# Kernel optimization log

Hardware: AMD Instinct MI355X
Metric: run time of the kernel (lower is better)

Reference implementation:

```python
import jax, jax.numpy as jnp
import numpy as np

D_MODEL = 1024
H = 4
DK = 128   # head_qk_dim (key_dim=512)
DV = 256   # head_v_dim (value_dim=1024)
EPS = 1e-5
SCALE = DK ** -0.5


def setup_inputs() -> dict:
    key = jax.random.key(0)
    ks = jax.random.split(key, 8)
    w = lambda k, i, o: jax.random.normal(k, (i, o), jnp.float32) * (2.0 ** -2.5) * (6.0 / (i + o)) ** 0.5 * 2
    return {
        "x": jax.random.normal(ks[0], (2, 4096, D_MODEL), jnp.float32),
        "Wq": w(ks[1], D_MODEL, H * DK),
        "Wk": w(ks[2], D_MODEL, H * DK),
        "Wv": w(ks[3], D_MODEL, H * DV),
        "Wb": w(ks[4], D_MODEL, H),
        "Wg": w(ks[5], D_MODEL, H * DV),
        "Wo": w(ks[6], H * DV, D_MODEL),
        "norm_w": jnp.ones((DV,), jnp.float32),
    }


def _delta_rule(q, k, v, beta):
    """Delta-rule linear attention. q,k: [b,n,h,dk], v: [b,n,h,dv], beta: [b,n,h].
    S_t = S_{t-1} + k_t (beta_t * (v_t - k_t^T S_{t-1}))^T ; o_t = q_t^T S_t."""
    b = q.shape[0]
    # time-major for scan: [n,b,h,*]
    qt = jnp.moveaxis(q, 1, 0)
    kt = jnp.moveaxis(k, 1, 0)
    vt = jnp.moveaxis(v, 1, 0)
    bt = jnp.moveaxis(beta, 1, 0)
    S0 = jnp.zeros((b, H, DK, DV), q.dtype)

    def step(S, inp):
        q_t, k_t, v_t, b_t = inp
        pred = jnp.einsum('bhk,bhkv->bhv', k_t, S)          # current memory readout
        delta = (v_t - pred) * b_t[..., None]                # beta-scaled error
        S = S + k_t[..., :, None] * delta[..., None, :]      # rank-1 update [b,h,dk,dv]
        o_t = jnp.einsum('bhk,bhkv->bhv', q_t, S)
        return S, o_t

    _, o = jax.lax.scan(step, S0, (qt, kt, vt, bt))          # o: [n,b,h,dv]
    return jnp.moveaxis(o, 0, 1)                             # [b,n,h,dv]


def reference(x, Wq, Wk, Wv, Wb, Wg, Wo, norm_w):
    b, n, _ = x.shape
    q = (x @ Wq).reshape(b, n, H, DK)
    k = (x @ Wk).reshape(b, n, H, DK)
    v = (x @ Wv).reshape(b, n, H, DV)
    beta = jax.nn.sigmoid(x @ Wb)                            # [b,n,h]
    # L2-normalize keys (delta-rule kernels assume unit-norm k) and scale q
    k = k * jax.lax.rsqrt(jnp.sum(k * k, axis=-1, keepdims=True) + 1e-12)
    q = q * SCALE
    o = _delta_rule(q, k, v, beta)                           # [b,n,h,dv]
    # FusedRMSNormSwishGate over head_v_dim
    g = (x @ Wg).reshape(b, n, H, DV)
    o = o * jax.lax.rsqrt(jnp.mean(o * o, axis=-1, keepdims=True) + EPS) * norm_w
    o = o * (g * jax.nn.sigmoid(g))                          # swish gate
    return o.reshape(b, n, H * DV) @ Wo
```

## Files before the change

kernel.cpp:

```cpp
#include <hip/hip_runtime.h>
#include <hip/hip_bf16.h>
#include <stdint.h>
#include <stddef.h>

typedef __attribute__((ext_vector_type(8))) short short8v;
typedef __attribute__((ext_vector_type(4))) float f32x4;
typedef unsigned short us;

__device__ __forceinline__ float bf2f(unsigned short u) {
    return __uint_as_float(((unsigned int)u) << 16);
}
__device__ __forceinline__ unsigned short f2bf(float f) {
    unsigned int x = __float_as_uint(f);
    x += 0x7fffu + ((x >> 16) & 1u);
    return (unsigned short)(x >> 16);
}
__device__ __forceinline__ unsigned int cvtpk(float lo, float hi) {
    unsigned int r;
    asm("v_cvt_pk_bf16_f32 %0, %1, %2" : "=v"(r) : "v"(lo), "v"(hi));
    return r;
}

#define NTOK 8192
#define DM   1024
#define NPROJ 3072
#define SEQ  4096
#define NCHUNK 64
#define SCQ 0.08838834764831845f

#define GLDS16(g, l) __builtin_amdgcn_global_load_lds( \
    (const __attribute__((address_space(1))) void*)(g), \
    (__attribute__((address_space(3))) void*)(l), 16, 0, 0)

__device__ __forceinline__ void bar_lgkm() {
    asm volatile("s_waitcnt lgkmcnt(0)" ::: "memory");
    __builtin_amdgcn_s_barrier();
    __builtin_amdgcn_sched_barrier(0);
}

__device__ __forceinline__ int sw16(int row, int k) {
    int u = k >> 3;
    int us_ = (u & 8) | ((u ^ row) & 7);
    return row * 128 + us_ * 8 + (k & 7);
}
__device__ __forceinline__ int sw8(int row, int k) {
    int u = k >> 3;
    int us_ = (u ^ row) & 7;
    return row * 64 + us_ * 8 + (k & 7);
}
__device__ __forceinline__ int sw128(int row, int k) {
    int u = k >> 3;
    return row * 128 + ((u ^ row) & 15) * 8 + (k & 7);
}
__device__ __forceinline__ int sw64(int row, int k) {
    int u = k >> 3;
    return row * 64 + ((u ^ row) & 7) * 8 + (k & 7);
}
__device__ __forceinline__ int sw64b(int row, int k) {
    int u = k >> 3;
    return row * 64 + ((u ^ row ^ (row >> 3)) & 7) * 8 + (k & 7);
}
__device__ __forceinline__ int swU(int t, int j) {
    int jj = j & 127, u = jj >> 3;
    int us_ = (u & 8) | ((u ^ t) & 7);
    return t * 256 + (j >> 7) * 128 + us_ * 8 + (jj & 7);
}
__device__ __forceinline__ int swU128(int t, int jj) {
    int u = jj >> 3;
    int us_ = (u & 8) | ((u ^ t) & 7);
    return t * 128 + us_ * 8 + (jj & 7);
}
__device__ __forceinline__ int sw64h(int row, int k) {
    int u = k >> 3;
    return row * 64 + ((u ^ row) & 7) * 8 + (k & 7);
}

__global__ void convert_x(const float* __restrict__ x, us* __restrict__ xb, int nunits) {
    int i = blockIdx.x * 256 + threadIdx.x;
    if (i >= nunits) return;
    int tok = i >> 7;
    int kb = (i >> 3) & 15;
    int u = i & 7;
    int ko = kb * 64 + ((u ^ (tok & 7)) * 8);
    const float4* src = (const float4*)(x + (size_t)tok * 1024 + ko);
    float4 v0 = src[0], v1 = src[1];
    uint4 o;
    o.x = cvtpk(v0.x, v0.y); o.y = cvtpk(v0.z, v0.w);
    o.z = cvtpk(v1.x, v1.y); o.w = cvtpk(v1.z, v1.w);
    *(uint4*)(xb + (size_t)i * 8) = o;
}

__global__ __launch_bounds__(256) void transpose_w(const float* __restrict__ src,
                                                   us* __restrict__ dst, int K, int N) {
    __shared__ float tl[64][65];
    int k0 = blockIdx.y * 64, n0 = blockIdx.x * 64;
    int tid = threadIdx.x;
    int tr = tid >> 6, tc = tid & 63;
    #pragma unroll
    for (int i = 0; i < 16; i++) {
        int kk = 4 * i + tr;
        tl[kk][tc] = src[(size_t)(k0 + kk) * N + n0 + tc];
    }
    __syncthreads();
    int n = tid >> 2, seg = (tid & 3) * 16;
    short8v a, b;
    #pragma unroll
    for (int e = 0; e < 8; e++) {
        a[e] = (short)f2bf(tl[seg + e][n]);
        b[e] = (short)f2bf(tl[seg + 8 + e][n]);
    }
    int n_ = n0 + n;
    int o1 = (tid & 3) * 2, o2_ = o1 + 1;
    us* d = dst + (size_t)n_ * K + k0;
    *(short8v*)(d + (o1 ^ (n_ & 7)) * 8) = a;
    *(short8v*)(d + (o2_ ^ (n_ & 7)) * 8) = b;
}

__global__ __launch_bounds__(256) void beta_kernel(const float* __restrict__ x,
                                                   const float* __restrict__ Wb,
                                                   float* __restrict__ beta) {
    __shared__ float part[16][16][4];
    int tl = threadIdx.x >> 4, sg = threadIdx.x & 15;
    int tok = blockIdx.x * 16 + tl;
    const float4* xr = (const float4*)(x + (size_t)tok * DM);
    const float4* wb = (const float4*)Wb;
    float s0 = 0.f, s1 = 0.f, s2 = 0.f, s3 = 0.f;
    #pragma unroll
    for (int it = 0; it < 16; it++) {
        int f = it * 16 + sg;
        float4 xv = xr[f];
        float4 w0 = wb[4 * f + 0], w1 = wb[4 * f + 1], w2 = wb[4 * f + 2], w3 = wb[4 * f + 3];
        s0 += xv.x * w0.x + xv.y * w1.x + xv.z * w2.x + xv.w * w3.x;
        s1 += xv.x * w0.y + xv.y * w1.y + xv.z * w2.y + xv.w * w3.y;
        s2 += xv.x * w0.z + xv.y * w1.z + xv.z * w2.z + xv.w * w3.z;
        s3 += xv.x * w0.w + xv.y * w1.w + xv.z * w2.w + xv.w * w3.w;
    }
    part[tl][sg][0] = s0; part[tl][sg][1] = s1; part[tl][sg][2] = s2; part[tl][sg][3] = s3;
    __syncthreads();
    if (threadIdx.x < 64) {
        int tl2 = threadIdx.x >> 2, h = threadIdx.x & 3;
        float s = 0.f;
        #pragma unroll
        for (int g = 0; g < 16; g++) s += part[tl2][g][h];
        beta[(size_t)(blockIdx.x * 16 + tl2) * 4 + h] = 1.f / (1.f + __expf(-s));
    }
}

template<int OUT_F32>
__global__ __launch_bounds__(256) void gemm_bt(
    const us* __restrict__ A, const us* __restrict__ BT,
    void* __restrict__ C, int M, int N, int K)
{
    __shared__ us As[128][64];
    __shared__ us Bs[128][64];
    int tid = threadIdx.x;
    int wave = tid >> 6, lane = tid & 63;
    int wr = (wave >> 1) * 64, wc = (wave & 1) * 64;
    int fr = lane & 15, fq = lane >> 4;
    int nbx = gridDim.x, nwg = nbx * gridDim.y;
    int wg = blockIdx.y * nbx + blockIdx.x;
    int cpx = nwg >> 3;
    wg = (wg & 7) * cpx + (wg >> 3);
    int m0 = (wg % nbx) * 128, n0 = (wg / nbx) * 128;

    f32x4 acc[4][4];
    #pragma unroll
    for (int i = 0; i < 4; i++)
        #pragma unroll
        for (int j = 0; j < 4; j++) acc[i][j] = (f32x4){0.f, 0.f, 0.f, 0.f};

    int rl = lane >> 3, ul = lane & 7;

    for (int k0 = 0; k0 < K; k0 += 64) {
        #pragma unroll
        for (int i = 0; i < 4; i++) {
            int row = wave * 32 + i * 8 + rl;
            GLDS16(&A[(size_t)(m0 + row) * K + k0 + ul * 8], &As[0][0] + (wave * 32 + i * 8) * 64);
            GLDS16(&BT[(size_t)(n0 + row) * K + k0 + ul * 8], &Bs[0][0] + (wave * 32 + i * 8) * 64);
        }
        __syncthreads();
        #pragma unroll
        for (int kk = 0; kk < 2; kk++) {
            short8v a[4], b[4];
            #pragma unroll
            for (int i = 0; i < 4; i++) {
                int ra = wr + i * 16 + fr;
                a[i] = *(const short8v*)&As[ra][((4 * kk + fq) ^ (ra & 7)) * 8];
                int rb = wc + i * 16 + fr;
                b[i] = *(const short8v*)&Bs[rb][((4 * kk + fq) ^ (rb & 7)) * 8];
            }
            #pragma unroll
            for (int i = 0; i < 4; i++)
                #pragma unroll
                for (int j = 0; j < 4; j++)
                    acc[i][j] = __builtin_amdgcn_mfma_f32_16x16x32_bf16(a[i], b[j], acc[i][j], 0, 0, 0);
        }
        __syncthreads();
    }
    #pragma unroll
    for (int i = 0; i < 4; i++)
        #pragma unroll
        for (int j = 0; j < 4; j++)
            #pragma unroll
            for (int t = 0; t < 4; t++) {
                int row = m0 + wr + i * 16 + fq * 4 + t;
                int col = n0 + wc + j * 16 + fr;
                float val = acc[i][j][t];
                if (OUT_F32) ((float*)C)[(size_t)row * N + col] = val;
                else ((us*)C)[(size_t)row * N + col] = f2bf(val);
            }
}

__global__ __launch_bounds__(256) void chunk_pre(
    const us* __restrict__ QKVG, const float* __restrict__ beta,
    us* __restrict__ Wbuf, us* __restrict__ Ubuf,
    us* __restrict__ Pbuf, us* __restrict__ KTbuf)
{
    __shared__ us Ks[8192];
    __shared__ us KTs[8192];
    __shared__ us VT[8192];
    __shared__ us Tb[4096];
    __shared__ float Af[64][64];
    __shared__ float betas[64];

    int c = blockIdx.x, bh = blockIdx.y;
    int b = bh >> 2, h = bh & 3;
    int tid = threadIdx.x;
    int wv = tid >> 6, ln = tid & 63;
    int fr = ln & 15, fq = ln >> 4;
    int tok0 = b * SEQ + c * 64;
    size_t cb = (size_t)bh * NCHUNK + c;

    #pragma unroll
    for (int r = 0; r < 4; r++) {
        int idx = tid + 256 * r;
        int t = idx >> 4, u = idx & 15;
        short8v kv = *(const short8v*)(QKVG + (size_t)(tok0 + t) * NPROJ + 512 + h * 128 + u * 8);
        *(short8v*)(Ks + sw16(t, u * 8)) = kv;
    }
    if (tid < 64) betas[tid] = beta[(size_t)(tok0 + tid) * 4 + h];
    __syncthreads();

    {
        int t = tid >> 2, p = tid & 3;
        short8v v[4];
        float ss = 0.f;
        #pragma unroll
        for (int uu = 0; uu < 4; uu++) {
            v[uu] = *(const short8v*)(Ks + sw16(t, (p * 4 + uu) * 8));
            #pragma unroll
            for (int e = 0; e < 8; e++) {
                float f = bf2f((unsigned short)v[uu][e]);
                ss += f * f;
            }
        }
        ss += __shfl_xor(ss, 1);
        ss += __shfl_xor(ss, 2);
        float rn = rsqrtf(ss + 1e-12f);
        #pragma unroll
        for (int uu = 0; uu < 4; uu++) {
            short8v o;
            #pragma unroll
            for (int e = 0; e < 8; e++)
                o[e] = (short)f2bf(bf2f((unsigned short)v[uu][e]) * rn);
            *(short8v*)(Ks + sw16(t, (p * 4 + uu) * 8)) = o;
        }
    }
    __syncthreads();

    {
        f32x4 aacc[4];
        #pragma unroll
        for (int jt = 0; jt < 4; jt++) aacc[jt] = (f32x4){0.f, 0.f, 0.f, 0.f};
        #pragma unroll
        for (int ks = 0; ks < 4; ks++) {
            short8v ak = *(const short8v*)(Ks + sw16(16 * wv + fr, 32 * ks + 8 * fq));
            #pragma unroll
            for (int jt = 0; jt < 4; jt++) {
                short8v bk = *(const short8v*)(Ks + sw16(16 * jt + fr, 32 * ks + 8 * fq));
                aacc[jt] = __builtin_amdgcn_mfma_f32_16x16x32_bf16(ak, bk, aacc[jt], 0, 0, 0);
            }
        }
        #pragma unroll
        for (int jt = 0; jt < 4; jt++)
            #pragma unroll
            for (int r = 0; r < 4; r++) {
                int t = 16 * wv + 4 * fq + r, s = 16 * jt + fr;
                if (s < t) Af[t][s] = betas[t] * aacc[jt][r];
            }
    }
    __syncthreads();

    if (wv == 0) {
        int cc = ln;
        for (int tb = 0; tb < 8; tb++) {
            int base = tb * 8;
            float xs[8];
            #pragma unroll
            for (int i = 0; i < 8; i++) {
                int t = base + i;
                float v = Af[t][cc];
                #pragma unroll
                for (int s = 0; s < i; s++)
                    v += Af[t][base + s] * xs[s];
                float xt = (cc < t) ? -v : 0.f;
                xs[i] = xt;
                if (cc < t) Af[t][cc] = xt;
            }
            for (int r = base + 8; r < 64; r += 2) {
                float u0 = 0.f, u1 = 0.f;
                #pragma unroll
                for (int s = 0; s < 8; s++) {
                    float a0 = Af[r][base + s];
                    float a1 = Af[r + 1][base + s];
                    u0 += a0 * xs[s];
                    u1 += a1 * xs[s];
                }
                Af[r][cc] += u0;
                Af[r + 1][cc] += u1;
            }
        }
    } else {
        int q = tid - 64;
        for (int g = q; g < 1024; g += 192) {
            int t = g >> 4, u = g & 15;
            short8v kv = *(const short8v*)(Ks + sw16(t, u * 8));
            #pragma unroll
            for (int e = 0; e < 8; e++)
                KTs[sw64b(u * 8 + e, t)] = (unsigned short)kv[e];
        }
        for (int g = q; g < 1024; g += 192) {
            int t = g >> 4, jg = g & 15;
            short8v vv = *(const short8v*)(QKVG + (size_t)(tok0 + t) * NPROJ + 1024 + h * 256 + jg * 8);
            #pragma unroll
            for (int e = 0; e < 8; e++)
                VT[sw64b(jg * 8 + e, t)] = (unsigned short)vv[e];
        }
    }
    __syncthreads();

    {
        f32x4 pacc[4];
        #pragma unroll
        for (int jt = 0; jt < 4; jt++) pacc[jt] = (f32x4){0.f, 0.f, 0.f, 0.f};
        #pragma unroll
        for (int ks = 0; ks < 4; ks++) {
            short8v aq = *(const short8v*)(QKVG + (size_t)(tok0 + 16 * wv + fr) * NPROJ + h * 128 + ks * 32 + fq * 8);
            #pragma unroll
            for (int jt = 0; jt < 4; jt++) {
                short8v bk = *(const short8v*)(Ks + sw16(16 * jt + fr, 32 * ks + 8 * fq));
                pacc[jt] = __builtin_amdgcn_mfma_f32_16x16x32_bf16(aq, bk, pacc[jt], 0, 0, 0);
            }
        }
        #pragma unroll
        for (int jt = 0; jt < 4; jt++)
            #pragma unroll
            for (int r = 0; r < 4; r++) {
                int t = 16 * wv + 4 * fq + r, s = 16 * jt + fr;
                float val = (s <= t) ? pacc[jt][r] * SCQ : 0.f;
                Pbuf[cb * 4096 + sw64(t, s)] = f2bf(val);
            }
        #pragma unroll
        for (int i = 0; i < 16; i++) {
            int idx = tid + 256 * i;
            int t = idx >> 6, s = idx & 63;
            float tv = (s < t) ? Af[t][s] : (s == t ? 1.f : 0.f);
            Tb[sw8(t, s)] = f2bf(tv * betas[s]);
        }
        #pragma unroll
        for (int i = 0; i < 4; i++) {
            int idx = tid + 256 * i;
            *(short8v*)(KTbuf + cb * 8192 + (size_t)idx * 8) =
                *(const short8v*)(KTs + (size_t)idx * 8);
        }
    }
    __syncthreads();

    {
        f32x4 wacc[8], uacc[8];
        #pragma unroll
        for (int jt = 0; jt < 8; jt++) {
            wacc[jt] = (f32x4){0.f, 0.f, 0.f, 0.f};
            uacc[jt] = (f32x4){0.f, 0.f, 0.f, 0.f};
        }
        #pragma unroll
        for (int ks = 0; ks < 2; ks++) {
            short8v at = *(const short8v*)(Tb + sw8(16 * wv + fr, 32 * ks + 8 * fq));
            #pragma unroll
            for (int jt = 0; jt < 8; jt++) {
                short8v bk = *(const short8v*)(KTs + sw64b(16 * jt + fr, 32 * ks + 8 * fq));
                wacc[jt] = __builtin_amdgcn_mfma_f32_16x16x32_bf16(at, bk, wacc[jt], 0, 0, 0);
                short8v bv = *(const short8v*)(VT + sw64b(16 * jt + fr, 32 * ks + 8 * fq));
                uacc[jt] = __builtin_amdgcn_mfma_f32_16x16x32_bf16(at, bv, uacc[jt], 0, 0, 0);
            }
        }
        #pragma unroll
        for (int jt = 0; jt < 8; jt++)
            #pragma unroll
            for (int r = 0; r < 4; r++) {
                int t = 16 * wv + 4 * fq + r, d = 16 * jt + fr;
                Wbuf[cb * 8192 + sw128(t, d)] = f2bf(-wacc[jt][r]);
                Ubuf[cb * 16384 + swU(t, d)] = f2bf(uacc[jt][r]);
            }
    }
    __syncthreads();

    #pragma unroll
    for (int i = 0; i < 4; i++) {
        int g = tid + 256 * i;
        int t = g >> 4, jg = g & 15;
        short8v vv = *(const short8v*)(QKVG + (size_t)(tok0 + t) * NPROJ + 1024 + h * 256 + 128 + jg * 8);
        #pragma unroll
        for (int e = 0; e < 8; e++)
            VT[sw64b(jg * 8 + e, t)] = (unsigned short)vv[e];
    }
    __syncthreads();
    {
        f32x4 uacc[8];
        #pragma unroll
        for (int jt = 0; jt < 8; jt++) uacc[jt] = (f32x4){0.f, 0.f, 0.f, 0.f};
        #pragma unroll
        for (int ks = 0; ks < 2; ks++) {
            short8v at = *(const short8v*)(Tb + sw8(16 * wv + fr, 32 * ks + 8 * fq));
            #pragma unroll
            for (int jt = 0; jt < 8; jt++) {
                short8v bv = *(const short8v*)(VT + sw64b(16 * jt + fr, 32 * ks + 8 * fq));
                uacc[jt] = __builtin_amdgcn_mfma_f32_16x16x32_bf16(at, bv, uacc[jt], 0, 0, 0);
            }
        }
        #pragma unroll
        for (int jt = 0; jt < 8; jt++)
            #pragma unroll
            for (int r = 0; r < 4; r++) {
                int t = 16 * wv + 4 * fq + r, j = 16 * jt + fr;
                Ubuf[cb * 16384 + swU(t, 128 + j)] = f2bf(uacc[jt][r]);
            }
    }
}

#define SCW 0
#define SCKT 8192
#define SCU 16384
#define SCBUF 17408
#define SCST 34816
#define SCDT 36864
#define SCPXB 77824

__global__ __launch_bounds__(128, 1) void scan_mfma(
    const us* __restrict__ Wbuf, const us* __restrict__ Ubuf,
    const us* __restrict__ KTbuf, us* __restrict__ Sbuf)
{
    extern __shared__ us lds[];
    float* pxf = (float*)((char*)lds + SCPXB);
    int tid = threadIdx.x;
    int wv = tid >> 6, ln = tid & 63;
    int fr = ln & 15, fq = ln >> 4;
    int sl = blockIdx.x;
    int j0 = sl * 16;
    int bh = blockIdx.y;

    short8v id0;
    #pragma unroll
    for (int e = 0; e < 8; e++)
        id0[e] = (short)((8 * fq + e == fr) ? 0x3F80 : 0);

    f32x4 sacc[4];
    #pragma unroll
    for (int i = 0; i < 4; i++) sacc[i] = (f32x4){0.f, 0.f, 0.f, 0.f};

    us* ST = lds + SCST + wv * 1024;
    us* DT = lds + SCDT + wv * 1024;

    auto issue = [&](int c1) {
        size_t cb = (size_t)bh * NCHUNK + c1;
        us* dst = lds + (c1 & 1) * SCBUF;
        const us* Wc = Wbuf + cb * 8192;
        const us* Kc = KTbuf + cb * 8192;
        #pragma unroll
        for (int i = 0; i < 8; i++) {
            int p = wv * 8 + i;
            GLDS16(Wc + p * 512 + ln * 8, dst + SCW + p * 512);
            GLDS16(Kc + wv * 4096 + i * 512 + ln * 8, dst + SCKT + wv * 4096 + i * 512);
        }
        const us* Uc = Ubuf + cb * 16384;
        int t = wv * 32 + (ln >> 1);
        GLDS16(Uc + swU(t, j0 + (ln & 1) * 8), dst + SCU + wv * 512);
    };

    issue(0);

    for (int c = 0; c < NCHUNK; c++) {
        const us* ba = lds + (c & 1) * SCBUF;

        #pragma unroll
        for (int dt = 0; dt < 4; dt++) {
            uint2 w;
            w.x = cvtpk(sacc[dt][0], sacc[dt][1]);
            w.y = cvtpk(sacc[dt][2], sacc[dt][3]);
            int dl = 16 * dt + 4 * fq;
            *(uint2*)&ST[fr * 64 + (((dl >> 3) ^ fr) & 7) * 8 + (dl & 7)] = w;
        }
        if (c + 1 < NCHUNK) issue(c + 1);
        {
            size_t sb = ((size_t)bh * NCHUNK + c) * 32768 + sl * 2048 + wv * 1024;
            #pragma unroll
            for (int q = 0; q < 2; q++) {
                short8v v = *(const short8v*)&ST[q * 512 + ln * 8];
                *(short8v*)(Sbuf + sb + q * 512 + ln * 8) = v;
            }
        }
        if (c + 1 < NCHUNK) {
            asm volatile("s_waitcnt vmcnt(19)" ::: "memory");
        } else {
            asm volatile("s_waitcnt vmcnt(4)" ::: "memory");
        }
        __builtin_amdgcn_sched_barrier(0);
        __builtin_amdgcn_s_barrier();
        __builtin_amdgcn_sched_barrier(0);

        f32x4 dacc[4];
        #pragma unroll
        for (int tt = 0; tt < 4; tt++) dacc[tt] = (f32x4){0.f, 0.f, 0.f, 0.f};
        #pragma unroll
        for (int kc = 0; kc < 2; kc++) {
            short8v bs = *(const short8v*)&ST[fr * 64 + (((4 * kc + fq) ^ fr) & 7) * 8];
            #pragma unroll
            for (int tt = 0; tt < 4; tt++) {
                short8v aw = *(const short8v*)&ba[SCW + sw128(16 * tt + fr, 64 * wv + 32 * kc + 8 * fq)];
                dacc[tt] = __builtin_amdgcn_mfma_f32_16x16x32_bf16(aw, bs, dacc[tt], 0, 0, 0);
            }
        }
        if (wv) {
            #pragma unroll
            for (int tt = 0; tt < 4; tt++) {
                short8v au = *(const short8v*)&ba[SCU + (16 * tt + fr) * 16 + 8 * (fq & 1)];
                dacc[tt] = __builtin_amdgcn_mfma_f32_16x16x32_bf16(au, id0, dacc[tt], 0, 0, 0);
            }
        }
        #pragma unroll
        for (int tt = 0; tt < 4; tt++)
            *(f32x4*)&pxf[wv * 1024 + tt * 256 + ln * 4] = dacc[tt];
        bar_lgkm();
        #pragma unroll
        for (int tt = 0; tt < 4; tt++) {
            f32x4 o = *(const f32x4*)&pxf[(wv ^ 1) * 1024 + tt * 256 + ln * 4];
            dacc[tt] += o;
        }
        #pragma unroll
        for (int tt = 0; tt < 4; tt++) {
            uint2 w;
            w.x = cvtpk(dacc[tt][0], dacc[tt][1]);
            w.y = cvtpk(dacc[tt][2], dacc[tt][3]);
            int tl = 16 * tt + 4 * fq;
            *(uint2*)&DT[fr * 64 + (((tl >> 3) ^ fr) & 7) * 8 + (tl & 7)] = w;
        }
        #pragma unroll
        for (int kc2 = 0; kc2 < 2; kc2++) {
            short8v bd = *(const short8v*)&DT[fr * 64 + (((4 * kc2 + fq) ^ fr) & 7) * 8];
            #pragma unroll
            for (int dt = 0; dt < 4; dt++) {
                short8v ak = *(const short8v*)&ba[SCKT + sw64b(64 * wv + 16 * dt + fr, 32 * kc2 + 8 * fq)];
                sacc[dt] = __builtin_amdgcn_mfma_f32_16x16x32_bf16(ak, bd, sacc[dt], 0, 0, 0);
            }
        }
    }
}

#define K2_W 0
#define K2_P 8192
#define K2_U 12288
#define K2_S 20480
#define K2_Q 36864
#define K2_DT 45056

__global__ __launch_bounds__(256, 1) void out_k(
    const us* __restrict__ QKVG, const us* __restrict__ Wbuf,
    const us* __restrict__ Ubuf, const us* __restrict__ Pbuf,
    const us* __restrict__ Sbuf, us* __restrict__ Ob)
{
    extern __shared__ us lds[];
    int tid = threadIdx.x;
    int wv = tid >> 6, ln = tid & 63;
    int fr = ln & 15, fq = ln >> 4;
    int c = blockIdx.x;
    int bh = blockIdx.y >> 1, jh = blockIdx.y & 1;
    int b = bh >> 2, h = bh & 3;
    int tok0 = b * SEQ + c * 64;
    size_t cb = (size_t)bh * NCHUNK + c;

    short8v id0, id1;
    #pragma unroll
    for (int e = 0; e < 8; e++) {
        id0[e] = (short)((8 * fq + e == fr) ? 0x3F80 : 0);
        id1[e] = (short)((8 * fq + e == fr + 16) ? 0x3F80 : 0);
    }

    #pragma unroll
    for (int i = 0; i < 4; i++) {
        int q = (i * 4 + wv) * 512 + ln * 8;
        GLDS16(Wbuf + cb * 8192 + q, lds + K2_W + (i * 4 + wv) * 512);
    }
    #pragma unroll
    for (int i = 0; i < 2; i++) {
        int q = (i * 4 + wv) * 512 + ln * 8;
        GLDS16(Pbuf + cb * 4096 + q, lds + K2_P + (i * 4 + wv) * 512);
    }
    #pragma unroll
    for (int i = 0; i < 4; i++) {
        int q = (i * 4 + wv) * 512 + ln * 8;
        int t = q >> 7, r = q & 127;
        GLDS16(Ubuf + cb * 16384 + t * 256 + jh * 128 + r, lds + K2_U + (i * 4 + wv) * 512);
    }
    size_t sbase = cb * 32768 + (size_t)jh * 16384;
    #pragma unroll
    for (int i = 0; i < 8; i++) {
        int q = (i * 4 + wv) * 512 + ln * 8;
        GLDS16(Sbuf + sbase + q, lds + K2_S + (i * 4 + wv) * 512);
    }
    short8v qv[4];
    #pragma unroll
    for (int i = 0; i < 4; i++) {
        int idx = tid + 256 * i;
        int t = idx >> 4, u = idx & 15;
        qv[i] = *(const short8v*)(QKVG + (size_t)(tok0 + t) * NPROJ + h * 128 + u * 8);
    }
    #pragma unroll
    for (int i = 0; i < 4; i++) {
        int idx = tid + 256 * i;
        int t = idx >> 4, u = idx & 15;
        *(short8v*)&lds[K2_Q + sw128(t, u * 8)] = qv[i];
    }
    __syncthreads();

    f32x4 dacc[8], oacc[8];
    #pragma unroll
    for (int jt = 0; jt < 8; jt++) {
        dacc[jt] = (f32x4){0.f, 0.f, 0.f, 0.f};
        oacc[jt] = (f32x4){0.f, 0.f, 0.f, 0.f};
    }
    #pragma unroll
    for (int ks = 0; ks < 4; ks++) {
        short8v aw = *(const short8v*)&lds[K2_W + sw128(16 * wv + fr, 32 * ks + 8 * fq)];
        short8v aq = *(const short8v*)&lds[K2_Q + sw128(16 * wv + fr, 32 * ks + 8 * fq)];
        #pragma unroll
        for (int jt = 0; jt < 8; jt++) {
            short8v bs = *(const short8v*)&lds[K2_S + jt * 2048 + (ks >> 1) * 1024
                + fr * 64 + ((((ks & 1) * 4 + fq) ^ fr) & 7) * 8];
            dacc[jt] = __builtin_amdgcn_mfma_f32_16x16x32_bf16(aw, bs, dacc[jt], 0, 0, 0);
            oacc[jt] = __builtin_amdgcn_mfma_f32_16x16x32_bf16(aq, bs, oacc[jt], 0, 0, 0);
        }
    }
    #pragma unroll
    for (int ju = 0; ju < 4; ju++) {
        short8v au = *(const short8v*)&lds[K2_U + swU128(16 * wv + fr, 32 * ju + 8 * fq)];
        dacc[2 * ju + 0] = __builtin_amdgcn_mfma_f32_16x16x32_bf16(au, id0, dacc[2 * ju + 0], 0, 0, 0);
        dacc[2 * ju + 1] = __builtin_amdgcn_mfma_f32_16x16x32_bf16(au, id1, dacc[2 * ju + 1], 0, 0, 0);
    }
    #pragma unroll
    for (int jt = 0; jt < 8; jt++)
        #pragma unroll
        for (int r = 0; r < 4; r++) oacc[jt][r] *= SCQ;
    #pragma unroll
    for (int jt = 0; jt < 8; jt++) {
        int j = 16 * jt + fr;
        int t0 = 16 * wv + 4 * fq;
        uint2 w;
        w.x = cvtpk(dacc[jt][0], dacc[jt][1]);
        w.y = cvtpk(dacc[jt][2], dacc[jt][3]);
        *(uint2*)&lds[K2_DT + sw64(j, t0)] = w;
    }
    bar_lgkm();

    #pragma unroll
    for (int ks = 0; ks < 2; ks++) {
        short8v ap = *(const short8v*)&lds[K2_P + sw64(16 * wv + fr, 32 * ks + 8 * fq)];
        #pragma unroll
        for (int jt = 0; jt < 8; jt++) {
            short8v bd = *(const short8v*)&lds[K2_DT + sw64(16 * jt + fr, 32 * ks + 8 * fq)];
            oacc[jt] = __builtin_amdgcn_mfma_f32_16x16x32_bf16(ap, bd, oacc[jt], 0, 0, 0);
        }
    }
    us* ob = Ob + (size_t)tok0 * 1024 + h * 256 + jh * 128;
    #pragma unroll
    for (int jt = 0; jt < 8; jt++)
        #pragma unroll
        for (int r = 0; r < 4; r++) {
            int t = 16 * wv + 4 * fq + r;
            ob[(size_t)t * 1024 + 16 * jt + fr] = f2bf(oacc[jt][r]);
        }
}

__global__ __launch_bounds__(256) void gate_norm(const us* __restrict__ Ob,
                                                 const us* __restrict__ QKVG,
                                                 const float* __restrict__ norm_w,
                                                 us* __restrict__ o2)
{
    int gid = blockIdx.x * 4 + (threadIdx.x >> 6);
    int ln = threadIdx.x & 63;
    int tok = gid >> 2, h = gid & 3;
    size_t base = (size_t)tok * 1024 + h * 256 + ln * 4;
    uint2 ov = *(const uint2*)&Ob[base];
    float o0 = bf2f((us)ov.x), o1 = bf2f((us)(ov.x >> 16));
    float o2v = bf2f((us)ov.y), o3 = bf2f((us)(ov.y >> 16));
    float ss = o0 * o0 + o1 * o1 + o2v * o2v + o3 * o3;
    #pragma unroll
    for (int off = 32; off; off >>= 1) ss += __shfl_xor(ss, off);
    float r = rsqrtf(ss * (1.0f / 256.0f) + 1e-5f);
    uint2 gv = *(const uint2*)&QKVG[(size_t)tok * NPROJ + 2048 + h * 256 + ln * 4];
    float g0 = bf2f((us)gv.x), g1 = bf2f((us)(gv.x >> 16));
    float g2 = bf2f((us)gv.y), g3 = bf2f((us)(gv.y >> 16));
    float4 nw = *(const float4*)&norm_w[ln * 4];
    float r0 = o0 * r * nw.x * (g0 / (1.f + __expf(-g0)));
    float r1 = o1 * r * nw.y * (g1 / (1.f + __expf(-g1)));
    float r2 = o2v * r * nw.z * (g2 / (1.f + __expf(-g2)));
    float r3 = o3 * r * nw.w * (g3 / (1.f + __expf(-g3)));
    uint2 w;
    w.x = cvtpk(r0, r1);
    w.y = cvtpk(r2, r3);
    int u = h * 32 + (ln >> 1);
    size_t dsto = (size_t)tok * 1024 + (size_t)(u >> 3) * 64
                + (size_t)(((u & 7) ^ (tok & 7)) * 8) + (ln & 1) * 4;
    *(uint2*)&o2[dsto] = w;
}

extern "C" void kernel_launch(void* const* d_in, const int* in_sizes, int n_in,
                              void* d_out, int out_size, void* d_ws, size_t ws_size,
                              hipStream_t stream) {
    const float* x      = (const float*)d_in[0];
    const float* Wq     = (const float*)d_in[1];
    const float* Wk     = (const float*)d_in[2];
    const float* Wv     = (const float*)d_in[3];
    const float* Wb     = (const float*)d_in[4];
    const float* Wg     = (const float*)d_in[5];
    const float* Wo     = (const float*)d_in[6];
    const float* norm_w = (const float*)d_in[7];
    float* out = (float*)d_out;

    char* ws = (char*)d_ws;
    us*    xb   = (us*)(ws + 0);
    us*    WT   = (us*)(ws + 16777216);
    us*    Sbuf = (us*)(ws + 0);
    us*    KTbuf= (us*)(ws + 33554432);
    us*    Ob   = (us*)(ws + 33554432);
    us*    QKVG = (us*)(ws + 50331648);
    float* beta = (float*)(ws + 100663296);
    us*    Wbuf = (us*)(ws + 100794368);
    us*    Ubuf = (us*)(ws + 109182976);
    us*    o2   = (us*)(ws + 109182976);
    us*    Pbuf = (us*)(ws + 125960192);
    us*    WoT  = (us*)(ws + 130154496);

    (void)hipFuncSetAttribute((const void*)scan_mfma,
                              hipFuncAttributeMaxDynamicSharedMemorySize, 86016);
    (void)hipFuncSetAttribute((const void*)out_k,
                              hipFuncAttributeMaxDynamicSharedMemorySize, 106496);

    convert_x<<<NTOK * 128 / 256, 256, 0, stream>>>(x, xb, NTOK * 128);
    transpose_w<<<dim3(8, 16), 256, 0, stream>>>(Wq, WT, DM, 512);
    transpose_w<<<dim3(8, 16), 256, 0, stream>>>(Wk, WT + (size_t)512 * DM, DM, 512);
    transpose_w<<<dim3(16, 16), 256, 0, stream>>>(Wv, WT + (size_t)1024 * DM, DM, 1024);
    transpose_w<<<dim3(16, 16), 256, 0, stream>>>(Wg, WT + (size_t)2048 * DM, DM, 1024);
    transpose_w<<<dim3(16, 16), 256, 0, stream>>>(Wo, WoT, DM, 1024);
    beta_kernel<<<NTOK / 16, 256, 0, stream>>>(x, Wb, beta);
    gemm_bt<0><<<dim3(64, 24), 256, 0, stream>>>(xb, WT, (void*)QKVG, NTOK, NPROJ, DM);
    chunk_pre<<<dim3(NCHUNK, 8), 256, 0, stream>>>(QKVG, beta, Wbuf, Ubuf, Pbuf, KTbuf);
    scan_mfma<<<dim3(16, 8), 128, 86016, stream>>>(Wbuf, Ubuf, KTbuf, Sbuf);
    out_k<<<dim3(NCHUNK, 16), 256, 106496, stream>>>(QKVG, Wbuf, Ubuf, Pbuf, Sbuf, Ob);
    gate_norm<<<NTOK, 256, 0, stream>>>(Ob, QKVG, norm_w, o2);
    gemm_bt<1><<<dim3(64, 8), 256, 0, stream>>>(o2, WoT, (void*)out, NTOK, DM, DM);
}
```

Measured before the change: 264.9 us.

## Precompute per-chunk transition matrix to shorten serial scan dependency chain

chunk_pre now also forms a per-chunk 128x128 matrix M = K^T W (stored as Mbuf), plus a transposed U layout, so the scan step becomes S_new = S + K^T U + M S without the intermediate D = W S + U round-trip through LDS and the cross-wave reduction. scan_mfma drops one barrier and the fp32 partial-sum exchange per chunk, writes S directly to global, and double-buffers the state tile. The cost is more work in chunk_pre, a larger Mbuf load per chunk in the scan (more LDS and bandwidth), and a changed grid mapping. out_k is adapted to the transposed U layout.

```diff
diff --git a/kernel.cpp b/kernel.cpp
--- a/kernel.cpp
+++ b/kernel.cpp
@@ -60,19 +60,9 @@
     int u = k >> 3;
     return row * 64 + ((u ^ row ^ (row >> 3)) & 7) * 8 + (k & 7);
 }
-__device__ __forceinline__ int swU(int t, int j) {
-    int jj = j & 127, u = jj >> 3;
-    int us_ = (u & 8) | ((u ^ t) & 7);
-    return t * 256 + (j >> 7) * 128 + us_ * 8 + (jj & 7);
-}
-__device__ __forceinline__ int swU128(int t, int jj) {
-    int u = jj >> 3;
-    int us_ = (u & 8) | ((u ^ t) & 7);
-    return t * 128 + us_ * 8 + (jj & 7);
-}
-__device__ __forceinline__ int sw64h(int row, int k) {
-    int u = k >> 3;
-    return row * 64 + ((u ^ row) & 7) * 8 + (k & 7);
+__device__ __forceinline__ int swUT(int j, int t) {
+    int u = t >> 3;
+    return j * 64 + ((u ^ j) & 7) * 8 + (t & 7);
 }
 
 __global__ void convert_x(const float* __restrict__ x, us* __restrict__ xb, int nunits) {
@@ -213,8 +203,8 @@
 
 __global__ __launch_bounds__(256) void chunk_pre(
     const us* __restrict__ QKVG, const float* __restrict__ beta,
-    us* __restrict__ Wbuf, us* __restrict__ Ubuf,
-    us* __restrict__ Pbuf, us* __restrict__ KTbuf)
+    us* __restrict__ Wbuf, us* __restrict__ UbufT,
+    us* __restrict__ Pbuf, us* __restrict__ KTbuf, us* __restrict__ Mbuf)
 {
     __shared__ us Ks[8192];
     __shared__ us KTs[8192];
@@ -222,6 +212,7 @@
     __shared__ us Tb[4096];
     __shared__ float Af[64][64];
     __shared__ float betas[64];
+    us* WTl = (us*)&Af[0][0];
 
     int c = blockIdx.x, bh = blockIdx.y;
     int b = bh >> 2, h = bh & 3;
@@ -399,8 +390,10 @@
             #pragma unroll
             for (int r = 0; r < 4; r++) {
                 int t = 16 * wv + 4 * fq + r, d = 16 * jt + fr;
-                Wbuf[cb * 8192 + sw128(t, d)] = f2bf(-wacc[jt][r]);
-                Ubuf[cb * 16384 + swU(t, d)] = f2bf(uacc[jt][r]);
+                us wneg = f2bf(-wacc[jt][r]);
+                Wbuf[cb * 8192 + sw128(t, d)] = wneg;
+                WTl[sw64b(d, t)] = wneg;
+                UbufT[cb * 16384 + swUT(d, t)] = f2bf(uacc[jt][r]);
             }
     }
     __syncthreads();
@@ -432,65 +425,81 @@
         for (int jt = 0; jt < 8; jt++)
             #pragma unroll
             for (int r = 0; r < 4; r++) {
-                int t = 16 * wv + 4 * fq + r, j = 16 * jt + fr;
-                Ubuf[cb * 16384 + swU(t, 128 + j)] = f2bf(uacc[jt][r]);
-            }
-    }
-}
-
-#define SCW 0
-#define SCKT 8192
-#define SCU 16384
-#define SCBUF 17408
-#define SCST 34816
-#define SCDT 36864
-#define SCPXB 77824
+                int t = 16 * wv + 4 * fq + r, j = 128 + 16 * jt + fr;
+                UbufT[cb * 16384 + swUT(j, t)] = f2bf(uacc[jt][r]);
+            }
+    }
+
+    {
+        #pragma unroll
+        for (int mw = 0; mw < 2; mw++) {
+            int mt = wv + 4 * mw;
+            f32x4 macc[8];
+            #pragma unroll
+            for (int nt = 0; nt < 8; nt++) macc[nt] = (f32x4){0.f, 0.f, 0.f, 0.f};
+            #pragma unroll
+            for (int ks = 0; ks < 2; ks++) {
+                short8v akt = *(const short8v*)(KTs + sw64b(16 * mt + fr, 32 * ks + 8 * fq));
+                #pragma unroll
+                for (int nt = 0; nt < 8; nt++) {
+                    short8v bwt = *(const short8v*)(WTl + sw64b(16 * nt + fr, 32 * ks + 8 * fq));
+                    macc[nt] = __builtin_amdgcn_mfma_f32_16x16x32_bf16(akt, bwt, macc[nt], 0, 0, 0);
+                }
+            }
+            #pragma unroll
+            for (int nt = 0; nt < 8; nt++)
+                #pragma unroll
+                for (int r = 0; r < 4; r++) {
+                    int d = 16 * mt + 4 * fq + r, dp = 16 * nt + fr;
+                    Mbuf[cb * 16384 + sw128(d, dp)] = f2bf(macc[nt][r]);
+                }
+        }
+    }
+}
+
+#define SMB 0
+#define SKT 16384
+#define SUT 24576
+#define SBUFSZ 25600
+#define SSTB (2 * SBUFSZ)
 
 __global__ __launch_bounds__(128, 1) void scan_mfma(
-    const us* __restrict__ Wbuf, const us* __restrict__ Ubuf,
+    const us* __restrict__ Mbuf, const us* __restrict__ UbufT,
     const us* __restrict__ KTbuf, us* __restrict__ Sbuf)
 {
     extern __shared__ us lds[];
-    float* pxf = (float*)((char*)lds + SCPXB);
     int tid = threadIdx.x;
     int wv = tid >> 6, ln = tid & 63;
     int fr = ln & 15, fq = ln >> 4;
-    int sl = blockIdx.x;
+    int sl = blockIdx.x >> 3;
     int j0 = sl * 16;
-    int bh = blockIdx.y;
-
-    short8v id0;
-    #pragma unroll
-    for (int e = 0; e < 8; e++)
-        id0[e] = (short)((8 * fq + e == fr) ? 0x3F80 : 0);
+    int bh = blockIdx.x & 7;
 
     f32x4 sacc[4];
     #pragma unroll
     for (int i = 0; i < 4; i++) sacc[i] = (f32x4){0.f, 0.f, 0.f, 0.f};
-
-    us* ST = lds + SCST + wv * 1024;
-    us* DT = lds + SCDT + wv * 1024;
 
     auto issue = [&](int c1) {
         size_t cb = (size_t)bh * NCHUNK + c1;
-        us* dst = lds + (c1 & 1) * SCBUF;
-        const us* Wc = Wbuf + cb * 8192;
-        const us* Kc = KTbuf + cb * 8192;
-        #pragma unroll
-        for (int i = 0; i < 8; i++) {
-            int p = wv * 8 + i;
-            GLDS16(Wc + p * 512 + ln * 8, dst + SCW + p * 512);
-            GLDS16(Kc + wv * 4096 + i * 512 + ln * 8, dst + SCKT + wv * 4096 + i * 512);
-        }
-        const us* Uc = Ubuf + cb * 16384;
-        int t = wv * 32 + (ln >> 1);
-        GLDS16(Uc + swU(t, j0 + (ln & 1) * 8), dst + SCU + wv * 512);
+        us* dst = lds + (c1 & 1) * SBUFSZ;
+        const us* Mc = Mbuf + cb * 16384 + wv * 8192;
+        const us* Kc = KTbuf + cb * 8192 + wv * 4096;
+        #pragma unroll
+        for (int i = 0; i < 16; i++)
+            GLDS16(Mc + i * 512 + ln * 8, dst + SMB + wv * 8192 + i * 512);
+        #pragma unroll
+        for (int i = 0; i < 8; i++)
+            GLDS16(Kc + i * 512 + ln * 8, dst + SKT + wv * 4096 + i * 512);
+        GLDS16(UbufT + cb * 16384 + j0 * 64 + wv * 512 + ln * 8, dst + SUT + wv * 512);
     };
 
     issue(0);
 
     for (int c = 0; c < NCHUNK; c++) {
-        const us* ba = lds + (c & 1) * SCBUF;
+        const us* ba = lds + (c & 1) * SBUFSZ;
+        us* STw = lds + SSTB + (c & 1) * 2048 + wv * 1024;
+        const us* STr = lds + SSTB + (c & 1) * 2048;
+        size_t sb = ((size_t)bh * NCHUNK + c) * 32768 + sl * 2048 + wv * 1024;
 
         #pragma unroll
         for (int dt = 0; dt < 4; dt++) {
@@ -498,69 +507,38 @@
             w.x = cvtpk(sacc[dt][0], sacc[dt][1]);
             w.y = cvtpk(sacc[dt][2], sacc[dt][3]);
             int dl = 16 * dt + 4 * fq;
-            *(uint2*)&ST[fr * 64 + (((dl >> 3) ^ fr) & 7) * 8 + (dl & 7)] = w;
+            int off = fr * 64 + (((dl >> 3) ^ fr) & 7) * 8 + (dl & 7);
+            *(uint2*)&STw[off] = w;
+            *(uint2*)(Sbuf + sb + off) = w;
         }
         if (c + 1 < NCHUNK) issue(c + 1);
-        {
-            size_t sb = ((size_t)bh * NCHUNK + c) * 32768 + sl * 2048 + wv * 1024;
-            #pragma unroll
-            for (int q = 0; q < 2; q++) {
-                short8v v = *(const short8v*)&ST[q * 512 + ln * 8];
-                *(short8v*)(Sbuf + sb + q * 512 + ln * 8) = v;
-            }
-        }
-        if (c + 1 < NCHUNK) {
-            asm volatile("s_waitcnt vmcnt(19)" ::: "memory");
+        if (c == 0) {
+            asm volatile("s_waitcnt vmcnt(29)" ::: "memory");
+        } else if (c + 1 < NCHUNK) {
+            asm volatile("s_waitcnt vmcnt(33)" ::: "memory");
         } else {
-            asm volatile("s_waitcnt vmcnt(4)" ::: "memory");
+            asm volatile("s_waitcnt vmcnt(8)" ::: "memory");
         }
         __builtin_amdgcn_sched_barrier(0);
-        __builtin_amdgcn_s_barrier();
-        __builtin_amdgcn_sched_barrier(0);
-
-        f32x4 dacc[4];
-        #pragma unroll
-        for (int tt = 0; tt < 4; tt++) dacc[tt] = (f32x4){0.f, 0.f, 0.f, 0.f};
-        #pragma unroll
-        for (int kc = 0; kc < 2; kc++) {
-            short8v bs = *(const short8v*)&ST[fr * 64 + (((4 * kc + fq) ^ fr) & 7) * 8];
-            #pragma unroll
-            for (int tt = 0; tt < 4; tt++) {
-                short8v aw = *(const short8v*)&ba[SCW + sw128(16 * tt + fr, 64 * wv + 32 * kc + 8 * fq)];
-                dacc[tt] = __builtin_amdgcn_mfma_f32_16x16x32_bf16(aw, bs, dacc[tt], 0, 0, 0);
-            }
-        }
-        if (wv) {
-            #pragma unroll
-            for (int tt = 0; tt < 4; tt++) {
-                short8v au = *(const short8v*)&ba[SCU + (16 * tt + fr) * 16 + 8 * (fq & 1)];
-                dacc[tt] = __builtin_amdgcn_mfma_f32_16x16x32_bf16(au, id0, dacc[tt], 0, 0, 0);
-            }
-        }
-        #pragma unroll
-        for (int tt = 0; tt < 4; tt++)
-            *(f32x4*)&pxf[wv * 1024 + tt * 256 + ln * 4] = dacc[tt];
         bar_lgkm();
-        #pragma unroll
-        for (int tt = 0; tt < 4; tt++) {
-            f32x4 o = *(const f32x4*)&pxf[(wv ^ 1) * 1024 + tt * 256 + ln * 4];
-            dacc[tt] += o;
-        }
-        #pragma unroll
-        for (int tt = 0; tt < 4; tt++) {
-            uint2 w;
-            w.x = cvtpk(dacc[tt][0], dacc[tt][1]);
-            w.y = cvtpk(dacc[tt][2], dacc[tt][3]);
-            int tl = 16 * tt + 4 * fq;
-            *(uint2*)&DT[fr * 64 + (((tl >> 3) ^ fr) & 7) * 8 + (tl & 7)] = w;
-        }
-        #pragma unroll
-        for (int kc2 = 0; kc2 < 2; kc2++) {
-            short8v bd = *(const short8v*)&DT[fr * 64 + (((4 * kc2 + fq) ^ fr) & 7) * 8];
+
+        #pragma unroll
+        for (int ks = 0; ks < 2; ks++) {
+            short8v but = *(const short8v*)&ba[SUT + fr * 64 + (((4 * ks + fq) ^ (fr & 7)) & 7) * 8];
             #pragma unroll
             for (int dt = 0; dt < 4; dt++) {
-                short8v ak = *(const short8v*)&ba[SCKT + sw64b(64 * wv + 16 * dt + fr, 32 * kc2 + 8 * fq)];
-                sacc[dt] = __builtin_amdgcn_mfma_f32_16x16x32_bf16(ak, bd, sacc[dt], 0, 0, 0);
+                short8v akt = *(const short8v*)&ba[SKT + wv * 4096 + sw64b(16 * dt + fr, 32 * ks + 8 * fq)];
+                sacc[dt] = __builtin_amdgcn_mfma_f32_16x16x32_bf16(akt, but, sacc[dt], 0, 0, 0);
+            }
+        }
+        #pragma unroll
+        for (int kc = 0; kc < 4; kc++) {
+            short8v bs = *(const short8v*)&STr[(kc >> 1) * 1024 + fr * 64
+                + ((((kc & 1) * 4 + fq) ^ fr) & 7) * 8];
+            #pragma unroll
+            for (int dt = 0; dt < 4; dt++) {
+                short8v am = *(const short8v*)&ba[SMB + sw128(64 * wv + 16 * dt + fr, 32 * kc + 8 * fq)];
+                sacc[dt] = __builtin_amdgcn_mfma_f32_16x16x32_bf16(am, bs, sacc[dt], 0, 0, 0);
             }
         }
     }
@@ -575,7 +553,7 @@
 
 __global__ __launch_bounds__(256, 1) void out_k(
     const us* __restrict__ QKVG, const us* __restrict__ Wbuf,
-    const us* __restrict__ Ubuf, const us* __restrict__ Pbuf,
+    const us* __restrict__ UbufT, const us* __restrict__ Pbuf,
     const us* __restrict__ Sbuf, us* __restrict__ Ob)
 {
     extern __shared__ us lds[];
@@ -588,12 +566,10 @@
     int tok0 = b * SEQ + c * 64;
     size_t cb = (size_t)bh * NCHUNK + c;
 
-    short8v id0, id1;
-    #pragma unroll
-    for (int e = 0; e < 8; e++) {
-        id0[e] = (short)((8 * fq + e == fr) ? 0x3F80 : 0);
-        id1[e] = (short)((8 * fq + e == fr + 16) ? 0x3F80 : 0);
-    }
+    short8v idw;
+    #pragma unroll
+    for (int e = 0; e < 8; e++)
+        idw[e] = (short)((8 * fq + e == fr + 16 * (wv & 1)) ? 0x3F80 : 0);
 
     #pragma unroll
     for (int i = 0; i < 4; i++) {
@@ -608,8 +584,7 @@
     #pragma unroll
     for (int i = 0; i < 4; i++) {
         int q = (i * 4 + wv) * 512 + ln * 8;
-        int t = q >> 7, r = q & 127;
-        GLDS16(Ubuf + cb * 16384 + t * 256 + jh * 128 + r, lds + K2_U + (i * 4 + wv) * 512);
+        GLDS16(UbufT + cb * 16384 + jh * 8192 + q, lds + K2_U + (i * 4 + wv) * 512);
     }
     size_t sbase = cb * 32768 + (size_t)jh * 16384;
     #pragma unroll
@@ -632,10 +607,10 @@
     }
     __syncthreads();
 
-    f32x4 dacc[8], oacc[8];
+    f32x4 daccT[8], oacc[8];
     #pragma unroll
     for (int jt = 0; jt < 8; jt++) {
-        dacc[jt] = (f32x4){0.f, 0.f, 0.f, 0.f};
+        daccT[jt] = (f32x4){0.f, 0.f, 0.f, 0.f};
         oacc[jt] = (f32x4){0.f, 0.f, 0.f, 0.f};
     }
     #pragma unroll
@@ -646,29 +621,27 @@
         for (int jt = 0; jt < 8; jt++) {
             short8v bs = *(const short8v*)&lds[K2_S + jt * 2048 + (ks >> 1) * 1024
                 + fr * 64 + ((((ks & 1) * 4 + fq) ^ fr) & 7) * 8];
-            dacc[jt] = __builtin_amdgcn_mfma_f32_16x16x32_bf16(aw, bs, dacc[jt], 0, 0, 0);
+            daccT[jt] = __builtin_amdgcn_mfma_f32_16x16x32_bf16(bs, aw, daccT[jt], 0, 0, 0);
             oacc[jt] = __builtin_amdgcn_mfma_f32_16x16x32_bf16(aq, bs, oacc[jt], 0, 0, 0);
         }
     }
     #pragma unroll
-    for (int ju = 0; ju < 4; ju++) {
-        short8v au = *(const short8v*)&lds[K2_U + swU128(16 * wv + fr, 32 * ju + 8 * fq)];
-        dacc[2 * ju + 0] = __builtin_amdgcn_mfma_f32_16x16x32_bf16(au, id0, dacc[2 * ju + 0], 0, 0, 0);
-        dacc[2 * ju + 1] = __builtin_amdgcn_mfma_f32_16x16x32_bf16(au, id1, dacc[2 * ju + 1], 0, 0, 0);
+    for (int jt = 0; jt < 8; jt++) {
+        short8v au = *(const short8v*)&lds[K2_U + (16 * jt + fr) * 64
+            + ((((wv >> 1) * 4 + fq) ^ (fr & 7)) & 7) * 8];
+        daccT[jt] = __builtin_amdgcn_mfma_f32_16x16x32_bf16(au, idw, daccT[jt], 0, 0, 0);
     }
     #pragma unroll
     for (int jt = 0; jt < 8; jt++)
         #pragma unroll
         for (int r = 0; r < 4; r++) oacc[jt][r] *= SCQ;
     #pragma unroll
-    for (int jt = 0; jt < 8; jt++) {
-        int j = 16 * jt + fr;
-        int t0 = 16 * wv + 4 * fq;
-        uint2 w;
-        w.x = cvtpk(dacc[jt][0], dacc[jt][1]);
-        w.y = cvtpk(dacc[jt][2], dacc[jt][3]);
-        *(uint2*)&lds[K2_DT + sw64(j, t0)] = w;
-    }
+    for (int jt = 0; jt < 8; jt++)
+        #pragma unroll
+        for (int r = 0; r < 4; r++) {
+            int j = 16 * jt + 4 * fq + r, t = 16 * wv + fr;
+            lds[K2_DT + sw64(j, t)] = f2bf(daccT[jt][r]);
+        }
     bar_lgkm();
 
     #pragma unroll
@@ -740,18 +713,19 @@
     us*    xb   = (us*)(ws + 0);
     us*    WT   = (us*)(ws + 16777216);
     us*    Sbuf = (us*)(ws + 0);
-    us*    KTbuf= (us*)(ws + 33554432);
+    us*    Mbuf = (us*)(ws + 33554432);
     us*    Ob   = (us*)(ws + 33554432);
     us*    QKVG = (us*)(ws + 50331648);
     float* beta = (float*)(ws + 100663296);
     us*    Wbuf = (us*)(ws + 100794368);
-    us*    Ubuf = (us*)(ws + 109182976);
+    us*    UbufT= (us*)(ws + 109182976);
     us*    o2   = (us*)(ws + 109182976);
     us*    Pbuf = (us*)(ws + 125960192);
     us*    WoT  = (us*)(ws + 130154496);
+    us*    KTbuf= (us*)(ws + 132251648);
 
     (void)hipFuncSetAttribute((const void*)scan_mfma,
-                              hipFuncAttributeMaxDynamicSharedMemorySize, 86016);
+                              hipFuncAttributeMaxDynamicSharedMemorySize, 110592);
     (void)hipFuncSetAttribute((const void*)out_k,
                               hipFuncAttributeMaxDynamicSharedMemorySize, 106496);
 
@@ -763,9 +737,9 @@
     transpose_w<<<dim3(16, 16), 256, 0, stream>>>(Wo, WoT, DM, 1024);
     beta_kernel<<<NTOK / 16, 256, 0, stream>>>(x, Wb, beta);
     gemm_bt<0><<<dim3(64, 24), 256, 0, stream>>>(xb, WT, (void*)QKVG, NTOK, NPROJ, DM);
-    chunk_pre<<<dim3(NCHUNK, 8), 256, 0, stream>>>(QKVG, beta, Wbuf, Ubuf, Pbuf, KTbuf);
-    scan_mfma<<<dim3(16, 8), 128, 86016, stream>>>(Wbuf, Ubuf, KTbuf, Sbuf);
-    out_k<<<dim3(NCHUNK, 16), 256, 106496, stream>>>(QKVG, Wbuf, Ubuf, Pbuf, Sbuf, Ob);
+    chunk_pre<<<dim3(NCHUNK, 8), 256, 0, stream>>>(QKVG, beta, Wbuf, UbufT, Pbuf, KTbuf, Mbuf);
+    scan_mfma<<<128, 128, 110592, stream>>>(Mbuf, UbufT, KTbuf, Sbuf);
+    out_k<<<dim3(NCHUNK, 16), 256, 106496, stream>>>(QKVG, Wbuf, UbufT, Pbuf, Sbuf, Ob);
     gate_norm<<<NTOK, 256, 0, stream>>>(Ob, QKVG, norm_w, o2);
     gemm_bt<1><<<dim3(64, 8), 256, 0, stream>>>(o2, WoT, (void*)out, NTOK, DM, DM);
 }
```

New measurement: 282.1 us. +6.5%, slower.

## Restructure scan kernel's inter-wave reduction to remove a barrier and fp32 exchange

Applied to the files above, without the earlier changes.

Changes the chunk W layout to two 64-column halves so each wave loads only its own half of W and K. The scan now writes both waves' bf16 partial D tiles into double-buffered LDS and lets each wave accumulate both partials with extra MFMAs. This replaces the fp32 partial-sum exchange, the extra barrier and the LDS round trip for the state store, which now goes straight from registers to global. Block indexing is flattened to a 1D grid. The trade-off is twice the MFMAs in the state update, and the partials are rounded to bf16 before they are summed.

```diff
diff --git a/kernel.cpp b/kernel.cpp
--- a/kernel.cpp
+++ b/kernel.cpp
@@ -69,10 +69,6 @@
     int u = jj >> 3;
     int us_ = (u & 8) | ((u ^ t) & 7);
     return t * 128 + us_ * 8 + (jj & 7);
-}
-__device__ __forceinline__ int sw64h(int row, int k) {
-    int u = k >> 3;
-    return row * 64 + ((u ^ row) & 7) * 8 + (k & 7);
 }
 
 __global__ void convert_x(const float* __restrict__ x, us* __restrict__ xb, int nunits) {
@@ -399,7 +395,7 @@
             #pragma unroll
             for (int r = 0; r < 4; r++) {
                 int t = 16 * wv + 4 * fq + r, d = 16 * jt + fr;
-                Wbuf[cb * 8192 + sw128(t, d)] = f2bf(-wacc[jt][r]);
+                Wbuf[cb * 8192 + (d >> 6) * 4096 + sw64(t, d & 63)] = f2bf(-wacc[jt][r]);
                 Ubuf[cb * 16384 + swU(t, d)] = f2bf(uacc[jt][r]);
             }
     }
@@ -442,22 +438,20 @@
 #define SCKT 8192
 #define SCU 16384
 #define SCBUF 17408
-#define SCST 34816
-#define SCDT 36864
-#define SCPXB 77824
+#define SSTB (2 * SCBUF)
+#define SDTB (2 * SCBUF + 2048)
 
 __global__ __launch_bounds__(128, 1) void scan_mfma(
     const us* __restrict__ Wbuf, const us* __restrict__ Ubuf,
     const us* __restrict__ KTbuf, us* __restrict__ Sbuf)
 {
     extern __shared__ us lds[];
-    float* pxf = (float*)((char*)lds + SCPXB);
     int tid = threadIdx.x;
     int wv = tid >> 6, ln = tid & 63;
     int fr = ln & 15, fq = ln >> 4;
-    int sl = blockIdx.x;
+    int sl = blockIdx.x >> 3;
     int j0 = sl * 16;
-    int bh = blockIdx.y;
+    int bh = blockIdx.x & 7;
 
     short8v id0;
     #pragma unroll
@@ -468,29 +462,35 @@
     #pragma unroll
     for (int i = 0; i < 4; i++) sacc[i] = (f32x4){0.f, 0.f, 0.f, 0.f};
 
-    us* ST = lds + SCST + wv * 1024;
-    us* DT = lds + SCDT + wv * 1024;
+    us* ST = lds + SSTB + wv * 1024;
 
     auto issue = [&](int c1) {
         size_t cb = (size_t)bh * NCHUNK + c1;
         us* dst = lds + (c1 & 1) * SCBUF;
-        const us* Wc = Wbuf + cb * 8192;
-        const us* Kc = KTbuf + cb * 8192;
+        const us* Wc = Wbuf + cb * 8192 + wv * 4096;
+        const us* Kc = KTbuf + cb * 8192 + wv * 4096;
         #pragma unroll
         for (int i = 0; i < 8; i++) {
-            int p = wv * 8 + i;
-            GLDS16(Wc + p * 512 + ln * 8, dst + SCW + p * 512);
-            GLDS16(Kc + wv * 4096 + i * 512 + ln * 8, dst + SCKT + wv * 4096 + i * 512);
-        }
-        const us* Uc = Ubuf + cb * 16384;
-        int t = wv * 32 + (ln >> 1);
-        GLDS16(Uc + swU(t, j0 + (ln & 1) * 8), dst + SCU + wv * 512);
+            GLDS16(Wc + i * 512 + ln * 8, dst + SCW + wv * 4096 + i * 512);
+            GLDS16(Kc + i * 512 + ln * 8, dst + SCKT + wv * 4096 + i * 512);
+        }
+        if (wv) {
+            const us* Uc = Ubuf + cb * 16384;
+            #pragma unroll
+            for (int i = 0; i < 2; i++) {
+                int t = i * 32 + (ln >> 1);
+                GLDS16(Uc + swU(t, j0 + (ln & 1) * 8), dst + SCU + i * 512);
+            }
+        }
     };
 
     issue(0);
 
     for (int c = 0; c < NCHUNK; c++) {
         const us* ba = lds + (c & 1) * SCBUF;
+        us* DTw = lds + SDTB + (c & 1) * 2048 + wv * 1024;
+        const us* DTr = lds + SDTB + (c & 1) * 2048;
+        size_t sb = ((size_t)bh * NCHUNK + c) * 32768 + sl * 2048 + wv * 1024;
 
         #pragma unroll
         for (int dt = 0; dt < 4; dt++) {
@@ -498,25 +498,18 @@
             w.x = cvtpk(sacc[dt][0], sacc[dt][1]);
             w.y = cvtpk(sacc[dt][2], sacc[dt][3]);
             int dl = 16 * dt + 4 * fq;
-            *(uint2*)&ST[fr * 64 + (((dl >> 3) ^ fr) & 7) * 8 + (dl & 7)] = w;
+            int off = fr * 64 + (((dl >> 3) ^ fr) & 7) * 8 + (dl & 7);
+            *(uint2*)&ST[off] = w;
+            *(uint2*)(Sbuf + sb + off) = w;
         }
         if (c + 1 < NCHUNK) issue(c + 1);
-        {
-            size_t sb = ((size_t)bh * NCHUNK + c) * 32768 + sl * 2048 + wv * 1024;
-            #pragma unroll
-            for (int q = 0; q < 2; q++) {
-                short8v v = *(const short8v*)&ST[q * 512 + ln * 8];
-                *(short8v*)(Sbuf + sb + q * 512 + ln * 8) = v;
-            }
-        }
         if (c + 1 < NCHUNK) {
-            asm volatile("s_waitcnt vmcnt(19)" ::: "memory");
+            if (wv) asm volatile("s_waitcnt vmcnt(22)" ::: "memory");
+            else    asm volatile("s_waitcnt vmcnt(20)" ::: "memory");
         } else {
             asm volatile("s_waitcnt vmcnt(4)" ::: "memory");
         }
         __builtin_amdgcn_sched_barrier(0);
-        __builtin_amdgcn_s_barrier();
-        __builtin_amdgcn_sched_barrier(0);
 
         f32x4 dacc[4];
         #pragma unroll
@@ -526,7 +519,7 @@
             short8v bs = *(const short8v*)&ST[fr * 64 + (((4 * kc + fq) ^ fr) & 7) * 8];
             #pragma unroll
             for (int tt = 0; tt < 4; tt++) {
-                short8v aw = *(const short8v*)&ba[SCW + sw128(16 * tt + fr, 64 * wv + 32 * kc + 8 * fq)];
+                short8v aw = *(const short8v*)&ba[SCW + wv * 4096 + sw64(16 * tt + fr, 32 * kc + 8 * fq)];
                 dacc[tt] = __builtin_amdgcn_mfma_f32_16x16x32_bf16(aw, bs, dacc[tt], 0, 0, 0);
             }
         }
@@ -536,15 +529,6 @@
                 short8v au = *(const short8v*)&ba[SCU + (16 * tt + fr) * 16 + 8 * (fq & 1)];
                 dacc[tt] = __builtin_amdgcn_mfma_f32_16x16x32_bf16(au, id0, dacc[tt], 0, 0, 0);
             }
-        }
-        #pragma unroll
-        for (int tt = 0; tt < 4; tt++)
-            *(f32x4*)&pxf[wv * 1024 + tt * 256 + ln * 4] = dacc[tt];
-        bar_lgkm();
-        #pragma unroll
-        for (int tt = 0; tt < 4; tt++) {
-            f32x4 o = *(const f32x4*)&pxf[(wv ^ 1) * 1024 + tt * 256 + ln * 4];
-            dacc[tt] += o;
         }
         #pragma unroll
         for (int tt = 0; tt < 4; tt++) {
@@ -552,15 +536,19 @@
             w.x = cvtpk(dacc[tt][0], dacc[tt][1]);
             w.y = cvtpk(dacc[tt][2], dacc[tt][3]);
             int tl = 16 * tt + 4 * fq;
-            *(uint2*)&DT[fr * 64 + (((tl >> 3) ^ fr) & 7) * 8 + (tl & 7)] = w;
-        }
+            *(uint2*)&DTw[fr * 64 + (((tl >> 3) ^ fr) & 7) * 8 + (tl & 7)] = w;
+        }
+        bar_lgkm();
         #pragma unroll
         for (int kc2 = 0; kc2 < 2; kc2++) {
-            short8v bd = *(const short8v*)&DT[fr * 64 + (((4 * kc2 + fq) ^ fr) & 7) * 8];
+            int o = fr * 64 + (((4 * kc2 + fq) ^ fr) & 7) * 8;
+            short8v bd0 = *(const short8v*)&DTr[o];
+            short8v bd1 = *(const short8v*)&DTr[1024 + o];
             #pragma unroll
             for (int dt = 0; dt < 4; dt++) {
                 short8v ak = *(const short8v*)&ba[SCKT + sw64b(64 * wv + 16 * dt + fr, 32 * kc2 + 8 * fq)];
-                sacc[dt] = __builtin_amdgcn_mfma_f32_16x16x32_bf16(ak, bd, sacc[dt], 0, 0, 0);
+                sacc[dt] = __builtin_amdgcn_mfma_f32_16x16x32_bf16(ak, bd0, sacc[dt], 0, 0, 0);
+                sacc[dt] = __builtin_amdgcn_mfma_f32_16x16x32_bf16(ak, bd1, sacc[dt], 0, 0, 0);
             }
         }
     }
@@ -640,7 +628,8 @@
     }
     #pragma unroll
     for (int ks = 0; ks < 4; ks++) {
-        short8v aw = *(const short8v*)&lds[K2_W + sw128(16 * wv + fr, 32 * ks + 8 * fq)];
+        short8v aw = *(const short8v*)&lds[K2_W + (ks >> 1) * 4096
+            + sw64(16 * wv + fr, (ks & 1) * 32 + 8 * fq)];
         short8v aq = *(const short8v*)&lds[K2_Q + sw128(16 * wv + fr, 32 * ks + 8 * fq)];
         #pragma unroll
         for (int jt = 0; jt < 8; jt++) {
@@ -751,7 +740,7 @@
     us*    WoT  = (us*)(ws + 130154496);
 
     (void)hipFuncSetAttribute((const void*)scan_mfma,
-                              hipFuncAttributeMaxDynamicSharedMemorySize, 86016);
+                              hipFuncAttributeMaxDynamicSharedMemorySize, 81920);
     (void)hipFuncSetAttribute((const void*)out_k,
                               hipFuncAttributeMaxDynamicSharedMemorySize, 106496);
 
@@ -764,7 +753,7 @@
     beta_kernel<<<NTOK / 16, 256, 0, stream>>>(x, Wb, beta);
     gemm_bt<0><<<dim3(64, 24), 256, 0, stream>>>(xb, WT, (void*)QKVG, NTOK, NPROJ, DM);
     chunk_pre<<<dim3(NCHUNK, 8), 256, 0, stream>>>(QKVG, beta, Wbuf, Ubuf, Pbuf, KTbuf);
-    scan_mfma<<<dim3(16, 8), 128, 86016, stream>>>(Wbuf, Ubuf, KTbuf, Sbuf);
+    scan_mfma<<<128, 128, 81920, stream>>>(Wbuf, Ubuf, KTbuf, Sbuf);
     out_k<<<dim3(NCHUNK, 16), 256, 106496, stream>>>(QKVG, Wbuf, Ubuf, Pbuf, Sbuf, Ob);
     gate_norm<<<NTOK, 256, 0, stream>>>(Ob, QKVG, norm_w, o2);
     gemm_bt<1><<<dim3(64, 8), 256, 0, stream>>>(o2, WoT, (void*)out, NTOK, DM, DM);
```

After: 274.1 us. +3.5%, slower.
